# Optimization experiments

Hardware: AMD Instinct MI355X
Metric: run time of the kernel (lower is better)

The kernel has to match this reference:

```python
import jax, jax.numpy as jnp
import numpy as np

STRIDE = 8
D_STATE = 16
D_CONV = 4
DT_RANK = 8
NB = 2            # mamba blocks per direction
B, F_IN, L_IN = 2, 256, 250
F_OUT = 128
KSIZE = 16
L_OUT = (L_IN - 1) * STRIDE + KSIZE   # 2008
D_INNER = 2 * F_OUT                   # 256
LN_EPS = 1e-5


def setup_inputs() -> dict:
    key = jax.random.key(0)
    ks = jax.random.split(key, 12)
    s = 0.05
    return {
        'x': jax.random.normal(ks[0], (B, F_IN, L_IN), jnp.float32),
        'skip': jax.random.normal(ks[1], (B, F_OUT, L_OUT), jnp.float32),
        'res_for': jnp.zeros((1,), jnp.float32),
        'res_back': jnp.zeros((1,), jnp.float32),
        'convT_w': jax.random.normal(ks[2], (F_IN, F_OUT, KSIZE), jnp.float32) * s,
        'convT_b': jnp.zeros((F_OUT,), jnp.float32),
        'fuse_w': jax.random.normal(ks[3], (F_OUT, 2 * F_OUT), jnp.float32) * s,
        'fuse_b': jnp.zeros((F_OUT,), jnp.float32),
        'norm_w': jnp.ones((2, NB, F_OUT), jnp.float32),
        'norm_b': jnp.zeros((2, NB, F_OUT), jnp.float32),
        'in_proj_w': jax.random.normal(ks[4], (2, NB, 2 * D_INNER, F_OUT), jnp.float32) * s,
        'conv_w': jax.random.normal(ks[5], (2, NB, D_INNER, 1, D_CONV), jnp.float32) * s,
        'conv_b': jnp.zeros((2, NB, D_INNER), jnp.float32),
        'x_proj_w': jax.random.normal(ks[6], (2, NB, DT_RANK + 2 * D_STATE, D_INNER), jnp.float32) * s,
        'dt_proj_w': jax.random.normal(ks[7], (2, NB, D_INNER, DT_RANK), jnp.float32) * s,
        'dt_proj_b': jax.random.uniform(ks[8], (2, NB, D_INNER), jnp.float32, -4.0, -2.0),
        'A_log': jnp.broadcast_to(jnp.log(jnp.arange(1, D_STATE + 1, dtype=jnp.float32)), (2, NB, D_INNER, D_STATE)) + jnp.zeros((2, NB, D_INNER, D_STATE), jnp.float32),
        'D_skip': jnp.ones((2, NB, D_INNER), jnp.float32),
        'out_proj_w': jax.random.normal(ks[9], (2, NB, F_OUT, D_INNER), jnp.float32) * s,
    }


def _layernorm(x, w, b):
    mu = x.mean(-1, keepdims=True)
    var = ((x - mu) ** 2).mean(-1, keepdims=True)
    return (x - mu) * jax.lax.rsqrt(var + LN_EPS) * w + b


def _mamba_mixer(x, p):
    # x: [B,L,D] -> [B,L,D]
    Bb, L, _ = x.shape
    xz = jnp.einsum('bld,ed->ble', x, p['in_proj_w'])          # [B,L,2*d_in]
    xc, z = xz[..., :D_INNER], xz[..., D_INNER:]
    # causal depthwise conv1d (pad left d_conv-1)
    conv = jax.lax.conv_general_dilated(
        xc.transpose(0, 2, 1), p['conv_w'], (1,), [(D_CONV - 1, 0)],
        feature_group_count=D_INNER, dimension_numbers=('NCH', 'OIH', 'NCH'))
    xc = jax.nn.silu(conv + p['conv_b'][None, :, None]).transpose(0, 2, 1)  # [B,L,d_in]
    xdbl = jnp.einsum('bld,ed->ble', xc, p['x_proj_w'])        # [B,L,dt_rank+2N]
    dt = xdbl[..., :DT_RANK]
    Bm = xdbl[..., DT_RANK:DT_RANK + D_STATE]                  # [B,L,N]
    Cm = xdbl[..., DT_RANK + D_STATE:]                         # [B,L,N]
    delta = jax.nn.softplus(jnp.einsum('blr,dr->bld', dt, p['dt_proj_w']) + p['dt_proj_b'])
    A = -jnp.exp(p['A_log'])                                   # [d_in,N]

    def step(h, inp):
        d_t, B_t, C_t, u_t = inp                               # [B,d_in],[B,N],[B,N],[B,d_in]
        dA = jnp.exp(d_t[..., None] * A)                       # [B,d_in,N]
        h = dA * h + (d_t * u_t)[..., None] * B_t[:, None, :]
        y = jnp.einsum('bdn,bn->bd', h, C_t)
        return h, y

    h0 = jnp.zeros((Bb, D_INNER, D_STATE), xc.dtype)
    _, ys = jax.lax.scan(step, h0, (delta.transpose(1, 0, 2), Bm.transpose(1, 0, 2),
                                    Cm.transpose(1, 0, 2), xc.transpose(1, 0, 2)))
    y = ys.transpose(1, 0, 2) + xc * p['D_skip']               # [B,L,d_in]
    y = y * jax.nn.silu(z)
    return jnp.einsum('bld,od->blo', y, p['out_proj_w'])


def _mamba_stack(xseq, params, d):
    # prenorm residual blocks, as in mamba_ssm Block (fused_add_norm=False, LayerNorm)
    residual = None
    for i in range(NB):
        p = {k: params[k][d, i] for k in ('norm_w', 'norm_b', 'in_proj_w', 'conv_w', 'conv_b',
                                          'x_proj_w', 'dt_proj_w', 'dt_proj_b', 'A_log', 'D_skip', 'out_proj_w')}
        residual = xseq if residual is None else xseq + residual
        xseq = _mamba_mixer(_layernorm(residual, p['norm_w'], p['norm_b']), p)
    return xseq + residual


def _conv_transpose1d(x, w, b, stride):
    # torch ConvTranspose1d: x [B,Cin,L], w [Cin,Cout,K]
    K = w.shape[-1]
    w_t = jnp.flip(w, -1).transpose(1, 0, 2)                   # [Cout,Cin,K]
    y = jax.lax.conv_general_dilated(x, w_t, (1,), [(K - 1, K - 1)],
                                     lhs_dilation=(stride,),
                                     dimension_numbers=('NCH', 'OIH', 'NCH'))
    return y + b[None, :, None]


def _forward(x, skip, convT_w, convT_b, fuse_w, fuse_b, params):
    h = jax.nn.silu(_conv_transpose1d(x, convT_w, convT_b, STRIDE))
    pad = skip.shape[2] - h.shape[2]
    if pad > 0:
        h = jnp.pad(h, ((0, 0), (0, 0), (0, pad)))
    h = jnp.concatenate([skip, h], axis=1)                     # [B,2*F_OUT,L]
    h = jax.nn.silu(jnp.einsum('bcl,oc->bol', h, fuse_w) + fuse_b[None, :, None])
    xs = h.transpose(0, 2, 1)                                  # [B,L,F_OUT]
    xf = _mamba_stack(xs, params, 0)
    xb = jnp.flip(_mamba_stack(jnp.flip(xs, 1), params, 1), 1)
    return (xf + xb).transpose(0, 2, 1)                        # [B,F_OUT,L]


def reference(x, skip, res_for, res_back, convT_w, convT_b, fuse_w, fuse_b,
              norm_w, norm_b, in_proj_w, conv_w, conv_b, x_proj_w,
              dt_proj_w, dt_proj_b, A_log, D_skip, out_proj_w):
    params = dict(norm_w=norm_w, norm_b=norm_b, in_proj_w=in_proj_w, conv_w=conv_w,
                  conv_b=conv_b, x_proj_w=x_proj_w, dt_proj_w=dt_proj_w, dt_proj_b=dt_proj_b,
                  A_log=A_log, D_skip=D_skip, out_proj_w=out_proj_w)
    return _forward(x, skip, convT_w, convT_b, fuse_w, fuse_b, params)
```

## Files before the change

kernel.cpp:

```cpp
#include <hip/hip_runtime.h>
#include <hip/hip_bf16.h>
#include <math.h>

#define B_    2
#define FIN_  256
#define LIN_  250
#define F_    128
#define K_    16
#define ST_   8
#define L_    2008
#define DI_   256
#define DS_   16
#define RK_   8
#define CV_   4
#define NBLK_ 2
#define NC_   32
#define CL_   63
#define RL_   ((size_t)B_ * L_)

__device__ __forceinline__ float silu_f(float x) {
    return x / (1.f + __expf(-x));
}
__device__ __forceinline__ float softplus_f(float x) {
    return (x > 20.f) ? x : log1pf(__expf(x));
}
__device__ __forceinline__ float dot4(float4 a, float4 b) {
    return a.x * b.x + a.y * b.y + a.z * b.z + a.w * b.w;
}

#define PREP_N (524288 + 32768 + 262144 + 262144 + 65536)
__global__ void prep_k(const float* __restrict__ convT_w, const float* __restrict__ fuse_w,
                       const float* __restrict__ in_proj, const float* __restrict__ out_proj,
                       const float* __restrict__ x_proj,
                       float* __restrict__ W2p, float* __restrict__ fwTp,
                       float* __restrict__ ipTp, float* __restrict__ opTp,
                       float* __restrict__ xpTp) {
    size_t g = (size_t)blockIdx.x * 256 + threadIdx.x;
    if (g >= PREP_N) return;
    if (g < 524288) {
        int ccq = g >> 12, rr = g & 4095;
        int po = rr >> 2, i = rr & 3;
        int cc = ccq * 4 + i;
        int p = po >> 7, o = po & 127;
        int c = cc & 255, k = (cc < 256) ? p : p + 8;
        W2p[g] = convT_w[(size_t)c * 2048 + o * 16 + k];
        return;
    }
    g -= 524288;
    if (g < 32768) {
        int cq = g >> 9, rr = g & 511;
        int o = rr >> 2, i = rr & 3;
        fwTp[g] = fuse_w[(size_t)o * 256 + cq * 4 + i];
        return;
    }
    g -= 32768;
    if (g < 262144) {
        int db = g >> 16, r = g & 65535;
        int cq = r >> 11, rr = r & 2047;
        int e = rr >> 2, i = rr & 3;
        ipTp[g] = in_proj[(size_t)db * 65536 + e * 128 + cq * 4 + i];
        return;
    }
    g -= 262144;
    if (g < 262144) {
        int db = g >> 15, r = g & 32767;
        int cq = r >> 9, rr = r & 511;
        int o = rr >> 2, i = rr & 3;
        opTp[g] = out_proj[(size_t)db * 32768 + o * 256 + cq * 4 + i];
        return;
    }
    g -= 262144;
    {
        int db = g >> 14, r = g & 16383;
        int cq = r >> 8, rr = r & 255;
        int e = rr >> 2, i = rr & 3;
        xpTp[g] = (e < 40) ? x_proj[(size_t)db * 10240 + e * 256 + cq * 4 + i] : 0.f;
    }
}

__global__ void __launch_bounds__(256) convt4_k(
        const float* __restrict__ x, const float* __restrict__ W2p,
        const float* __restrict__ bias, float* __restrict__ hT) {
    int j0 = blockIdx.x * 4, nt = blockIdx.y, b = blockIdx.z;
    int po = nt * 256 + threadIdx.x;
    int p = po >> 7, o = po & 127;

    __shared__ float xr[5][264];

    for (int idx = threadIdx.x; idx < 5 * 256; idx += 256) {
        int i = idx >> 8, c = idx & 255;
        int j = j0 - 1 + i;
        xr[i][c] = (j >= 0 && j < LIN_) ? x[((size_t)b * FIN_ + c) * LIN_ + j] : 0.f;
    }
    __syncthreads();

    float acc[4] = {0.f, 0.f, 0.f, 0.f};
    const float4* W4 = (const float4*)W2p;

    for (int ccq = 0; ccq < 64; ++ccq) {
        float4 w1 = W4[(size_t)ccq * 1024 + po];
        float4 w2 = W4[(size_t)(ccq + 64) * 1024 + po];
        float4 xv[5];
        #pragma unroll
        for (int i = 0; i < 5; ++i) xv[i] = *(const float4*)&xr[i][ccq * 4];
        #pragma unroll
        for (int jj = 0; jj < 4; ++jj)
            acc[jj] += dot4(xv[jj + 1], w1) + dot4(xv[jj], w2);
    }
    float bo = bias[o];
    #pragma unroll
    for (int jj = 0; jj < 4; ++jj) {
        int j = j0 + jj;
        if (j <= 250) {
            int t = 8 * j + p;
            hT[((size_t)b * L_ + t) * F_ + o] = silu_f(acc[jj] + bo);
        }
    }
}

__global__ void __launch_bounds__(256) fuse4_k(
        const float* __restrict__ skip, const float* __restrict__ hT,
        const float* __restrict__ fwTp, const float* __restrict__ fb,
        float* __restrict__ xs) {
    int l0 = blockIdx.x * 8, b = blockIdx.y;
    int tid = threadIdx.x;

    __shared__ float ss[8][264];

    for (int idx = tid; idx < 128 * 8; idx += 256) {
        int c = idx >> 3, ll = idx & 7;
        ss[ll][c] = skip[((size_t)b * F_ + c) * L_ + l0 + ll];
    }
    for (int idx = tid; idx < 8 * 128; idx += 256) {
        int ll = idx >> 7, c = idx & 127;
        ss[ll][128 + c] = hT[((size_t)b * L_ + l0 + ll) * F_ + c];
    }
    __syncthreads();

    int o = tid & 127, lh = tid >> 7;
    float acc[4] = {0.f, 0.f, 0.f, 0.f};
    const float4* W4 = (const float4*)fwTp;

    for (int cq = 0; cq < 64; ++cq) {
        float4 w = W4[cq * 128 + o];
        #pragma unroll
        for (int rr = 0; rr < 4; ++rr)
            acc[rr] += dot4(*(const float4*)&ss[lh * 4 + rr][cq * 4], w);
    }
    float bo = fb[o];
    #pragma unroll
    for (int rr = 0; rr < 4; ++rr) {
        int l = l0 + lh * 4 + rr;
        float v = silu_f(acc[rr] + bo);
        xs[((size_t)b * L_ + l) * F_ + o] = v;
        xs[(RL_ + (size_t)b * L_ + (L_ - 1 - l)) * F_ + o] = v;
    }
}

__global__ void __launch_bounds__(256) ln4_k(
        const float* __restrict__ X, const float* __restrict__ nw,
        const float* __restrict__ nb_, const float* __restrict__ ipTp,
        float* __restrict__ XZ, int blk) {
    int rt = blockIdx.x, nt = blockIdx.y, d = blockIdx.z;
    int n0 = nt * 128;
    size_t rbase = (size_t)rt * 32;
    int tid = threadIdx.x, lane = tid & 63, wid = tid >> 6;
    int db = d * NBLK_ + blk;

    __shared__ float us[32][132];

    int wi0 = db * F_;
    for (int rr = 0; rr < 8; ++rr) {
        int r = wid * 8 + rr;
        size_t row = rbase + r;
        float2 v = make_float2(0.f, 0.f);
        if (row < RL_)
            v = *(const float2*)(X + ((size_t)d * RL_ + row) * F_ + lane * 2);
        float s1 = v.x + v.y, s2 = v.x * v.x + v.y * v.y;
        for (int off = 32; off; off >>= 1) {
            s1 += __shfl_xor(s1, off);
            s2 += __shfl_xor(s2, off);
        }
        float mu = s1 * (1.f / F_);
        float var = s2 * (1.f / F_) - mu * mu;
        float rstd = rsqrtf(var + 1e-5f);
        int c = lane * 2;
        us[r][c]     = (v.x - mu) * rstd * nw[wi0 + c]     + nb_[wi0 + c];
        us[r][c + 1] = (v.y - mu) * rstd * nw[wi0 + c + 1] + nb_[wi0 + c + 1];
    }
    __syncthreads();

    int o = tid & 127, rh = tid >> 7;
    float acc[16];
    #pragma unroll
    for (int i = 0; i < 16; ++i) acc[i] = 0.f;
    const float4* W4 = (const float4*)(ipTp + (size_t)db * 65536);

    for (int cq = 0; cq < 32; ++cq) {
        float4 w = W4[cq * 512 + n0 + o];
        #pragma unroll
        for (int rr = 0; rr < 16; ++rr)
            acc[rr] += dot4(*(const float4*)&us[rh * 16 + rr][cq * 4], w);
    }
    for (int rr = 0; rr < 16; ++rr) {
        size_t row = rbase + rh * 16 + rr;
        if (row < RL_)
            XZ[((size_t)d * RL_ + row) * (2 * DI_) + n0 + o] = acc[rr];
    }
}

__global__ void __launch_bounds__(256) dwxdt_k(
        const float* __restrict__ XZ, const float* __restrict__ cw,
        const float* __restrict__ cb, const float* __restrict__ xpTp,
        const float* __restrict__ dtw, const float* __restrict__ dtb,
        float* __restrict__ XC, float* __restrict__ BCM,
        float* __restrict__ DELTA, int blk) {
    int rt = blockIdx.x, d = blockIdx.y;
    int tid = threadIdx.x;
    size_t rbase = (size_t)rt * 16;
    int db = d * NBLK_ + blk;

    __shared__ float xzs[19][264];
    __shared__ float xcs[16][264];
    __shared__ float dts[16][8];

    for (int idx = tid; idx < 19 * 256; idx += 256) {
        int s = idx >> 8;
        int c = idx & 255;
        long g = (long)rbase - 3 + s;
        xzs[s][c] = (g >= 0) ? XZ[((size_t)d * RL_ + g) * (2 * DI_) + c] : 0.f;
    }
    __syncthreads();

    {
        int ch = tid;
        int wi = db * DI_ + ch;
        float w0 = cw[(size_t)wi * CV_ + 0], w1 = cw[(size_t)wi * CV_ + 1];
        float w2 = cw[(size_t)wi * CV_ + 2], w3 = cw[(size_t)wi * CV_ + 3];
        float bias = cb[wi];
        #pragma unroll 4
        for (int r = 0; r < 16; ++r) {
            size_t row = rbase + r;
            int b = (row >= L_) ? 1 : 0;
            int l = (int)(row - (size_t)b * L_);
            int s = r + 3;
            float acc = bias + xzs[s][ch] * w3;
            if (l - 1 >= 0) acc += xzs[s - 1][ch] * w2;
            if (l - 2 >= 0) acc += xzs[s - 2][ch] * w1;
            if (l - 3 >= 0) acc += xzs[s - 3][ch] * w0;
            float v = silu_f(acc);
            xcs[r][ch] = v;
            XC[((size_t)d * RL_ + row) * DI_ + ch] = v;
        }
    }
    __syncthreads();

    {
        int e = tid & 63, rg = tid >> 6;
        float acc[4] = {0.f, 0.f, 0.f, 0.f};
        const float4* W4 = (const float4*)(xpTp + (size_t)db * 16384);
        for (int cq = 0; cq < 64; ++cq) {
            float4 w = W4[cq * 64 + e];
            #pragma unroll
            for (int rr = 0; rr < 4; ++rr)
                acc[rr] += dot4(*(const float4*)&xcs[rg * 4 + rr][cq * 4], w);
        }
        if (e < RK_) {
            #pragma unroll
            for (int rr = 0; rr < 4; ++rr) dts[rg * 4 + rr][e] = acc[rr];
        } else if (e < RK_ + 2 * DS_) {
            #pragma unroll
            for (int rr = 0; rr < 4; ++rr) {
                size_t row = rbase + rg * 4 + rr;
                BCM[((size_t)d * RL_ + row) * 32 + (e - RK_)] = acc[rr];
            }
        }
    }
    __syncthreads();

    {
        int ch = tid;
        int wi = db * DI_ + ch;
        float dwv[RK_];
        #pragma unroll
        for (int k = 0; k < RK_; ++k) dwv[k] = dtw[(size_t)wi * RK_ + k];
        float bias = dtb[wi];
        #pragma unroll 4
        for (int rr = 0; rr < 16; ++rr) {
            size_t row = rbase + rr;
            float acc = bias;
            #pragma unroll
            for (int k = 0; k < RK_; ++k) acc += dts[rr][k] * dwv[k];
            DELTA[((size_t)d * RL_ + row) * DI_ + ch] = softplus_f(acc);
        }
    }
}

__global__ void __launch_bounds__(256) scanA_k(
        float* __restrict__ DELTA, const float* __restrict__ XC,
        const float* __restrict__ BCM, const float* __restrict__ A_log,
        float* __restrict__ Y, float* __restrict__ hpart,
        float* __restrict__ dsum, int blk) {
    int d = blockIdx.z, cnk = blockIdx.y;
    int chunit0 = blockIdx.x * 16;
    int chl = threadIdx.x >> 4, n = threadIdx.x & 15;
    int b = chunit0 >> 8, ch0 = chunit0 & 255;
    int ch = ch0 + chl;
    int t0 = cnk * CL_;
    int nt = L_ - t0 < CL_ ? L_ - t0 : CL_;

    __shared__ float dt_s[CL_][16];
    __shared__ float u_s[CL_][16];
    __shared__ float bc_s[CL_][32];

    size_t rowbase = (size_t)d * RL_ + (size_t)b * L_ + t0;
    for (int idx = threadIdx.x; idx < CL_ * 16; idx += 256) {
        int t = idx >> 4, c = idx & 15;
        float dv = 0.f, uv = 0.f;
        if (t < nt) {
            dv = DELTA[(rowbase + t) * DI_ + ch0 + c];
            uv = XC[(rowbase + t) * DI_ + ch0 + c];
        }
        dt_s[t][c] = dv; u_s[t][c] = uv;
    }
    for (int idx = threadIdx.x; idx < CL_ * 32; idx += 256) {
        int t = idx >> 5, m = idx & 31;
        bc_s[t][m] = (t < nt) ? BCM[(rowbase + t) * 32 + m] : 0.f;
    }
    __syncthreads();

    float A = -__expf(A_log[((size_t)(d * NBLK_ + blk) * DI_ + ch) * DS_ + n]);
    float h = 0.f, cum = 0.f;
    for (int t = 0; t < nt; ++t) {
        float dt = dt_s[t][chl];
        float u  = u_s[t][chl];
        float Bt = bc_s[t][n];
        float Ct = bc_s[t][16 + n];
        cum += dt;
        h = __expf(dt * A) * h + dt * u * Bt;
        float yp = h * Ct;
        yp += __shfl_xor(yp, 1);
        yp += __shfl_xor(yp, 2);
        yp += __shfl_xor(yp, 4);
        yp += __shfl_xor(yp, 8);
        if (n == 0) {
            Y[(rowbase + t) * DI_ + ch] = yp;
            DELTA[(rowbase + t) * DI_ + ch] = cum;
        }
    }
    size_t cb = (size_t)(d * B_ + b) * NC_ + cnk;
    hpart[cb * (DI_ * DS_) + ch * DS_ + n] = h;
    if (n == 0) dsum[cb * DI_ + ch] = cum;
}

__global__ void scanB_k(float* __restrict__ hpart, const float* __restrict__ dsum,
                        const float* __restrict__ A_log, int blk) {
    int d = blockIdx.y;
    int idx = blockIdx.x * 256 + threadIdx.x;
    int b = idx >> 12, ch = (idx >> 4) & 255, n = idx & 15;
    float A = -__expf(A_log[((size_t)(d * NBLK_ + blk) * DI_ + ch) * DS_ + n]);
    float h = 0.f;
    for (int c = 0; c < NC_; ++c) {
        size_t cb = (size_t)(d * B_ + b) * NC_ + c;
        size_t hi = cb * (DI_ * DS_) + ch * DS_ + n;
        float hc = hpart[hi];
        hpart[hi] = h;
        h = __expf(A * dsum[cb * DI_ + ch]) * h + hc;
    }
}

__global__ void __launch_bounds__(256) fixD_k(
        const float* __restrict__ DELTA , const float* __restrict__ BCM,
        const float* __restrict__ A_log, const float* __restrict__ hcarry,
        float* __restrict__ Y, int blk) {
    int d = blockIdx.z, cnk = blockIdx.y + 1;
    int chunit0 = blockIdx.x * 16;
    int b = chunit0 >> 8, ch0 = chunit0 & 255;
    int chl = threadIdx.x & 15, tg = threadIdx.x >> 4;
    int ch = ch0 + chl;
    int t0 = cnk * CL_;
    int nt = L_ - t0 < CL_ ? L_ - t0 : CL_;

    __shared__ float cum_s[CL_][17];
    __shared__ float c_s[CL_][17];
    __shared__ float hin_s[16][16];

    size_t rowbase = (size_t)d * RL_ + (size_t)b * L_ + t0;
    for (int idx = threadIdx.x; idx < CL_ * 16; idx += 256) {
        int t = idx >> 4, c = idx & 15;
        float cv = 0.f, Cv = 0.f;
        if (t < nt) {
            cv = DELTA[(rowbase + t) * DI_ + ch0 + c];
            Cv = BCM[(rowbase + t) * 32 + 16 + c];
        }
        cum_s[t][c] = cv; c_s[t][c] = Cv;
    }
    {
        size_t cb = ((size_t)(d * B_ + b) * NC_ + cnk) * (DI_ * DS_);
        int cl = threadIdx.x >> 4, n = threadIdx.x & 15;
        hin_s[cl][n] = hcarry[cb + (ch0 + cl) * DS_ + n];
    }
    __syncthreads();

    float An[16], Kn[16];
    const float* Ab = A_log + ((size_t)(d * NBLK_ + blk) * DI_ + ch) * DS_;
    #pragma unroll
    for (int n = 0; n < 16; ++n) {
        An[n] = -__expf(Ab[n]);
        Kn[n] = hin_s[chl][n];
    }
    #pragma unroll
    for (int tt = 0; tt < 4; ++tt) {
        int t = tg * 4 + tt;
        if (t < nt) {
            float cum = cum_s[t][chl];
            float corr = 0.f;
            #pragma unroll
            for (int n = 0; n < 16; ++n)
                corr += c_s[t][n] * Kn[n] * __expf(An[n] * cum);
            Y[(rowbase + t) * DI_ + ch] += corr;
        }
    }
}

__global__ void __launch_bounds__(256) gate4_k(
        const float* __restrict__ Y, const float* __restrict__ XC,
        const float* __restrict__ XZ, const float* __restrict__ Dsk,
        const float* __restrict__ opTp, const float* __restrict__ resid_in,
        float* __restrict__ outp, int blk) {
    int rt = blockIdx.x, d = blockIdx.y;
    int tid = threadIdx.x;
    size_t rbase = (size_t)rt * 16;
    int db = d * NBLK_ + blk;

    __shared__ float yg[16][264];

    {
        int c = tid;
        float Dc = Dsk[(size_t)db * DI_ + c];
        #pragma unroll 4
        for (int r = 0; r < 16; ++r) {
            size_t ri = (size_t)d * RL_ + rbase + r;
            float z = XZ[ri * (2 * DI_) + DI_ + c];
            yg[r][c] = (Y[ri * DI_ + c] + XC[ri * DI_ + c] * Dc) * silu_f(z);
        }
    }
    __syncthreads();

    int o = tid & 127, rh = tid >> 7;
    float acc[8];
    #pragma unroll
    for (int i = 0; i < 8; ++i) acc[i] = 0.f;
    const float4* W4 = (const float4*)(opTp + (size_t)db * 32768);

    for (int cq = 0; cq < 64; ++cq) {
        float4 w = W4[cq * 128 + o];
        #pragma unroll
        for (int rr = 0; rr < 8; ++rr)
            acc[rr] += dot4(*(const float4*)&yg[rh * 8 + rr][cq * 4], w);
    }
    for (int rr = 0; rr < 8; ++rr) {
        size_t row = rbase + rh * 8 + rr;
        size_t ri = (size_t)d * RL_ + row;
        float v = acc[rr];
        if (resid_in) v += resid_in[ri * F_ + o];
        outp[ri * F_ + o] = v;
    }
}

__global__ void combine2_k(const float* __restrict__ cur, const float* __restrict__ res1,
                           float* __restrict__ out) {
    int l0 = blockIdx.x * 64, b = blockIdx.y;
    int tid = threadIdx.x;
    __shared__ float s[64][129];
    for (int idx = tid; idx < 64 * 128; idx += 256) {
        int ll = idx >> 7, o = idx & 127;
        int l = l0 + ll;
        if (l < L_) {
            size_t rf = ((size_t)b * L_ + l) * F_ + o;
            size_t rb = (RL_ + (size_t)b * L_ + (L_ - 1 - l)) * F_ + o;
            s[ll][o] = cur[rf] + res1[rf] + cur[rb] + res1[rb];
        }
    }
    __syncthreads();
    for (int idx = tid; idx < 64 * 128; idx += 256) {
        int o = idx >> 6, ll = idx & 63;
        int l = l0 + ll;
        if (l < L_) out[((size_t)b * F_ + o) * L_ + l] = s[ll][o];
    }
}

extern "C" void kernel_launch(void* const* d_in, const int* in_sizes, int n_in,
                              void* d_out, int out_size, void* d_ws, size_t ws_size,
                              hipStream_t stream) {
    const float* x        = (const float*)d_in[0];
    const float* skip     = (const float*)d_in[1];
    const float* convT_w  = (const float*)d_in[4];
    const float* convT_b  = (const float*)d_in[5];
    const float* fuse_w   = (const float*)d_in[6];
    const float* fuse_b   = (const float*)d_in[7];
    const float* norm_w   = (const float*)d_in[8];
    const float* norm_b   = (const float*)d_in[9];
    const float* in_proj  = (const float*)d_in[10];
    const float* conv_w   = (const float*)d_in[11];
    const float* conv_b   = (const float*)d_in[12];
    const float* x_proj   = (const float*)d_in[13];
    const float* dt_projw = (const float*)d_in[14];
    const float* dt_projb = (const float*)d_in[15];
    const float* A_log    = (const float*)d_in[16];
    const float* D_skip   = (const float*)d_in[17];
    const float* out_proj = (const float*)d_in[18];
    float* out = (float*)d_out;

    float* w = (float*)d_ws;
    size_t off = 0;
    auto alloc = [&](size_t n) { float* p = w + off; off += n; return p; };
    float* hT      = alloc((size_t)B_ * L_ * F_);
    float* W2p     = alloc(524288);
    float* fwTp    = alloc(32768);
    float* ipTp    = alloc(262144);
    float* opTp    = alloc(262144);
    float* xpTp    = alloc(65536);
    float* xs      = alloc(2 * RL_ * F_);
    float* cur     = alloc(2 * RL_ * F_);
    float* res1    = alloc(2 * RL_ * F_);
    float* xz      = alloc(2 * RL_ * (2 * DI_));
    float* xc      = alloc(2 * RL_ * DI_);
    float* dl      = alloc(2 * RL_ * DI_);
    float* bcm     = alloc(2 * RL_ * 32);
    float* yb      = alloc(2 * RL_ * DI_);
    float* hp   = hT;
    float* dsum = hT + 524288;
    (void)ws_size; (void)in_sizes; (void)n_in; (void)out_size;

    prep_k<<<(PREP_N + 255) / 256, 256, 0, stream>>>(convT_w, fuse_w, in_proj, out_proj,
                                                     x_proj, W2p, fwTp, ipTp, opTp, xpTp);
    convt4_k<<<dim3(63, 4, 2), 256, 0, stream>>>(x, W2p, convT_b, hT);
    fuse4_k<<<dim3(251, 2), 256, 0, stream>>>(skip, hT, fwTp, fuse_b, xs);

    for (int blk = 0; blk < NBLK_; ++blk) {
        const float* Xin = (blk == 0) ? xs : res1;
        ln4_k<<<dim3(126, 4, 2), 256, 0, stream>>>(Xin, norm_w, norm_b, ipTp, xz, blk);
        dwxdt_k<<<dim3(251, 2), 256, 0, stream>>>(xz, conv_w, conv_b, xpTp,
                                                  dt_projw, dt_projb, xc, bcm, dl, blk);
        scanA_k<<<dim3(32, NC_, 2), 256, 0, stream>>>(dl, xc, bcm, A_log, yb, hp, dsum, blk);
        scanB_k<<<dim3(32, 2), 256, 0, stream>>>(hp, dsum, A_log, blk);
        fixD_k<<<dim3(32, NC_ - 1, 2), 256, 0, stream>>>(dl, bcm, A_log, hp, yb, blk);
        if (blk == 0)
            gate4_k<<<dim3(251, 2), 256, 0, stream>>>(yb, xc, xz, D_skip, opTp, xs, res1, 0);
        else
            gate4_k<<<dim3(251, 2), 256, 0, stream>>>(yb, xc, xz, D_skip, opTp, nullptr, cur, 1);
    }

    combine2_k<<<dim3(32, 2), 256, 0, stream>>>(cur, res1, out);
}
```

Baseline: 454.2 us.

## Re-tile GEMM kernels to multiple outputs per thread and double scan chunk count

The convT, fuse, LN+in_proj and gate GEMM kernels now compute two or four output columns per thread, so each shared-memory activation load is reused across more weights. The LN kernel now produces all 512 in_proj outputs per block over 16 rows instead of splitting N across grid.y, which removes the repeated LayerNorm work. The scan chunking goes from 32 chunks of 63 steps to 64 chunks of 32 steps, shortening the serial per-chunk work but making the carry pass longer. The dsum scratch buffer is moved into `cur` to fit the larger carry arrays, which is safe only because `cur` is written later, and more accumulators per thread raise register pressure.

```diff
diff --git a/kernel.cpp b/kernel.cpp
--- a/kernel.cpp
+++ b/kernel.cpp
@@ -14,8 +14,8 @@
 #define RK_   8
 #define CV_   4
 #define NBLK_ 2
-#define NC_   32
-#define CL_   63
+#define NC_   64
+#define CL_   32
 #define RL_   ((size_t)B_ * L_)
 
 __device__ __forceinline__ float silu_f(float x) {
@@ -78,11 +78,11 @@
     }
 }
 
-__global__ void __launch_bounds__(256) convt4_k(
+__global__ void __launch_bounds__(256) convt5_k(
         const float* __restrict__ x, const float* __restrict__ W2p,
         const float* __restrict__ bias, float* __restrict__ hT) {
     int j0 = blockIdx.x * 4, nt = blockIdx.y, b = blockIdx.z;
-    int po = nt * 256 + threadIdx.x;
+    int po = nt * 512 + threadIdx.x;
     int p = po >> 7, o = po & 127;
 
     __shared__ float xr[5][264];
@@ -94,31 +94,36 @@
     }
     __syncthreads();
 
-    float acc[4] = {0.f, 0.f, 0.f, 0.f};
+    float acca[4] = {0.f, 0.f, 0.f, 0.f};
+    float accb[4] = {0.f, 0.f, 0.f, 0.f};
     const float4* W4 = (const float4*)W2p;
 
     for (int ccq = 0; ccq < 64; ++ccq) {
-        float4 w1 = W4[(size_t)ccq * 1024 + po];
-        float4 w2 = W4[(size_t)(ccq + 64) * 1024 + po];
+        float4 wa1 = W4[(size_t)ccq * 1024 + po];
+        float4 wb1 = W4[(size_t)ccq * 1024 + po + 256];
+        float4 wa2 = W4[(size_t)(ccq + 64) * 1024 + po];
+        float4 wb2 = W4[(size_t)(ccq + 64) * 1024 + po + 256];
         float4 xv[5];
         #pragma unroll
         for (int i = 0; i < 5; ++i) xv[i] = *(const float4*)&xr[i][ccq * 4];
         #pragma unroll
-        for (int jj = 0; jj < 4; ++jj)
-            acc[jj] += dot4(xv[jj + 1], w1) + dot4(xv[jj], w2);
+        for (int jj = 0; jj < 4; ++jj) {
+            acca[jj] += dot4(xv[jj + 1], wa1) + dot4(xv[jj], wa2);
+            accb[jj] += dot4(xv[jj + 1], wb1) + dot4(xv[jj], wb2);
+        }
     }
     float bo = bias[o];
     #pragma unroll
     for (int jj = 0; jj < 4; ++jj) {
         int j = j0 + jj;
         if (j <= 250) {
-            int t = 8 * j + p;
-            hT[((size_t)b * L_ + t) * F_ + o] = silu_f(acc[jj] + bo);
-        }
-    }
-}
-
-__global__ void __launch_bounds__(256) fuse4_k(
+            hT[((size_t)b * L_ + 8 * j + p) * F_ + o]     = silu_f(acca[jj] + bo);
+            hT[((size_t)b * L_ + 8 * j + p + 2) * F_ + o] = silu_f(accb[jj] + bo);
+        }
+    }
+}
+
+__global__ void __launch_bounds__(256) fuse5_k(
         const float* __restrict__ skip, const float* __restrict__ hT,
         const float* __restrict__ fwTp, const float* __restrict__ fb,
         float* __restrict__ xs) {
@@ -137,45 +142,50 @@
     }
     __syncthreads();
 
-    int o = tid & 127, lh = tid >> 7;
-    float acc[4] = {0.f, 0.f, 0.f, 0.f};
+    int o2 = tid & 63, rg = tid >> 6;
+    float acca[2] = {0.f, 0.f}, accb[2] = {0.f, 0.f};
     const float4* W4 = (const float4*)fwTp;
 
     for (int cq = 0; cq < 64; ++cq) {
-        float4 w = W4[cq * 128 + o];
+        float4 wa = W4[cq * 128 + o2];
+        float4 wb = W4[cq * 128 + o2 + 64];
         #pragma unroll
-        for (int rr = 0; rr < 4; ++rr)
-            acc[rr] += dot4(*(const float4*)&ss[lh * 4 + rr][cq * 4], w);
-    }
-    float bo = fb[o];
-    #pragma unroll
-    for (int rr = 0; rr < 4; ++rr) {
-        int l = l0 + lh * 4 + rr;
-        float v = silu_f(acc[rr] + bo);
-        xs[((size_t)b * L_ + l) * F_ + o] = v;
-        xs[(RL_ + (size_t)b * L_ + (L_ - 1 - l)) * F_ + o] = v;
-    }
-}
-
-__global__ void __launch_bounds__(256) ln4_k(
+        for (int rr = 0; rr < 2; ++rr) {
+            float4 s = *(const float4*)&ss[rg * 2 + rr][cq * 4];
+            acca[rr] += dot4(s, wa);
+            accb[rr] += dot4(s, wb);
+        }
+    }
+    float ba = fb[o2], bb = fb[o2 + 64];
+    #pragma unroll
+    for (int rr = 0; rr < 2; ++rr) {
+        int l = l0 + rg * 2 + rr;
+        float va = silu_f(acca[rr] + ba);
+        float vb = silu_f(accb[rr] + bb);
+        size_t rf = ((size_t)b * L_ + l) * F_;
+        size_t rb = (RL_ + (size_t)b * L_ + (L_ - 1 - l)) * F_;
+        xs[rf + o2] = va;       xs[rf + o2 + 64] = vb;
+        xs[rb + o2] = va;       xs[rb + o2 + 64] = vb;
+    }
+}
+
+__global__ void __launch_bounds__(256) ln5_k(
         const float* __restrict__ X, const float* __restrict__ nw,
         const float* __restrict__ nb_, const float* __restrict__ ipTp,
         float* __restrict__ XZ, int blk) {
-    int rt = blockIdx.x, nt = blockIdx.y, d = blockIdx.z;
-    int n0 = nt * 128;
-    size_t rbase = (size_t)rt * 32;
+    int rt = blockIdx.x, d = blockIdx.y;
+    size_t rbase = (size_t)rt * 16;
     int tid = threadIdx.x, lane = tid & 63, wid = tid >> 6;
     int db = d * NBLK_ + blk;
 
-    __shared__ float us[32][132];
+    __shared__ float us[16][132];
 
     int wi0 = db * F_;
-    for (int rr = 0; rr < 8; ++rr) {
-        int r = wid * 8 + rr;
+    #pragma unroll
+    for (int rr = 0; rr < 4; ++rr) {
+        int r = wid * 4 + rr;
         size_t row = rbase + r;
-        float2 v = make_float2(0.f, 0.f);
-        if (row < RL_)
-            v = *(const float2*)(X + ((size_t)d * RL_ + row) * F_ + lane * 2);
+        float2 v = *(const float2*)(X + ((size_t)d * RL_ + row) * F_ + lane * 2);
         float s1 = v.x + v.y, s2 = v.x * v.x + v.y * v.y;
         for (int off = 32; off; off >>= 1) {
             s1 += __shfl_xor(s1, off);
@@ -191,21 +201,33 @@
     __syncthreads();
 
     int o = tid & 127, rh = tid >> 7;
-    float acc[16];
-    #pragma unroll
-    for (int i = 0; i < 16; ++i) acc[i] = 0.f;
+    float acc0[8], acc1[8], acc2[8], acc3[8];
+    #pragma unroll
+    for (int i = 0; i < 8; ++i) { acc0[i] = acc1[i] = acc2[i] = acc3[i] = 0.f; }
     const float4* W4 = (const float4*)(ipTp + (size_t)db * 65536);
 
     for (int cq = 0; cq < 32; ++cq) {
-        float4 w = W4[cq * 512 + n0 + o];
+        float4 w0 = W4[cq * 512 + o];
+        float4 w1 = W4[cq * 512 + o + 128];
+        float4 w2 = W4[cq * 512 + o + 256];
+        float4 w3 = W4[cq * 512 + o + 384];
         #pragma unroll
-        for (int rr = 0; rr < 16; ++rr)
-            acc[rr] += dot4(*(const float4*)&us[rh * 16 + rr][cq * 4], w);
-    }
-    for (int rr = 0; rr < 16; ++rr) {
-        size_t row = rbase + rh * 16 + rr;
-        if (row < RL_)
-            XZ[((size_t)d * RL_ + row) * (2 * DI_) + n0 + o] = acc[rr];
+        for (int rr = 0; rr < 8; ++rr) {
+            float4 u = *(const float4*)&us[rh * 8 + rr][cq * 4];
+            acc0[rr] += dot4(u, w0);
+            acc1[rr] += dot4(u, w1);
+            acc2[rr] += dot4(u, w2);
+            acc3[rr] += dot4(u, w3);
+        }
+    }
+    #pragma unroll
+    for (int rr = 0; rr < 8; ++rr) {
+        size_t row = rbase + rh * 8 + rr;
+        float* dst = XZ + ((size_t)d * RL_ + row) * (2 * DI_);
+        dst[o]       = acc0[rr];
+        dst[o + 128] = acc1[rr];
+        dst[o + 256] = acc2[rr];
+        dst[o + 384] = acc3[rr];
     }
 }
 
@@ -307,7 +329,7 @@
     int b = chunit0 >> 8, ch0 = chunit0 & 255;
     int ch = ch0 + chl;
     int t0 = cnk * CL_;
-    int nt = L_ - t0 < CL_ ? L_ - t0 : CL_;
+    int nt = L_ - t0; if (nt > CL_) nt = CL_;
 
     __shared__ float dt_s[CL_][16];
     __shared__ float u_s[CL_][16];
@@ -379,7 +401,7 @@
     int chl = threadIdx.x & 15, tg = threadIdx.x >> 4;
     int ch = ch0 + chl;
     int t0 = cnk * CL_;
-    int nt = L_ - t0 < CL_ ? L_ - t0 : CL_;
+    int nt = L_ - t0; if (nt > CL_) nt = CL_;
 
     __shared__ float cum_s[CL_][17];
     __shared__ float c_s[CL_][17];
@@ -397,8 +419,8 @@
     }
     {
         size_t cb = ((size_t)(d * B_ + b) * NC_ + cnk) * (DI_ * DS_);
-        int cl = threadIdx.x >> 4, n = threadIdx.x & 15;
-        hin_s[cl][n] = hcarry[cb + (ch0 + cl) * DS_ + n];
+        int cl = threadIdx.x >> 4, nn = threadIdx.x & 15;
+        hin_s[cl][nn] = hcarry[cb + (ch0 + cl) * DS_ + nn];
     }
     __syncthreads();
 
@@ -410,8 +432,8 @@
         Kn[n] = hin_s[chl][n];
     }
     #pragma unroll
-    for (int tt = 0; tt < 4; ++tt) {
-        int t = tg * 4 + tt;
+    for (int tt = 0; tt < 2; ++tt) {
+        int t = tg * 2 + tt;
         if (t < nt) {
             float cum = cum_s[t][chl];
             float corr = 0.f;
@@ -423,7 +445,7 @@
     }
 }
 
-__global__ void __launch_bounds__(256) gate4_k(
+__global__ void __launch_bounds__(256) gate5_k(
         const float* __restrict__ Y, const float* __restrict__ XC,
         const float* __restrict__ XZ, const float* __restrict__ Dsk,
         const float* __restrict__ opTp, const float* __restrict__ resid_in,
@@ -447,24 +469,31 @@
     }
     __syncthreads();
 
-    int o = tid & 127, rh = tid >> 7;
-    float acc[8];
-    #pragma unroll
-    for (int i = 0; i < 8; ++i) acc[i] = 0.f;
+    int o2 = tid & 63, rg = tid >> 6;
+    float acca[4] = {0.f, 0.f, 0.f, 0.f};
+    float accb[4] = {0.f, 0.f, 0.f, 0.f};
     const float4* W4 = (const float4*)(opTp + (size_t)db * 32768);
 
     for (int cq = 0; cq < 64; ++cq) {
-        float4 w = W4[cq * 128 + o];
+        float4 wa = W4[cq * 128 + o2];
+        float4 wb = W4[cq * 128 + o2 + 64];
         #pragma unroll
-        for (int rr = 0; rr < 8; ++rr)
-            acc[rr] += dot4(*(const float4*)&yg[rh * 8 + rr][cq * 4], w);
-    }
-    for (int rr = 0; rr < 8; ++rr) {
-        size_t row = rbase + rh * 8 + rr;
-        size_t ri = (size_t)d * RL_ + row;
-        float v = acc[rr];
-        if (resid_in) v += resid_in[ri * F_ + o];
-        outp[ri * F_ + o] = v;
+        for (int rr = 0; rr < 4; ++rr) {
+            float4 u = *(const float4*)&yg[rg * 4 + rr][cq * 4];
+            acca[rr] += dot4(u, wa);
+            accb[rr] += dot4(u, wb);
+        }
+    }
+    #pragma unroll
+    for (int rr = 0; rr < 4; ++rr) {
+        size_t ri = (size_t)d * RL_ + rbase + rg * 4 + rr;
+        float va = acca[rr], vb = accb[rr];
+        if (resid_in) {
+            va += resid_in[ri * F_ + o2];
+            vb += resid_in[ri * F_ + o2 + 64];
+        }
+        outp[ri * F_ + o2]      = va;
+        outp[ri * F_ + o2 + 64] = vb;
     }
 }
 
@@ -530,26 +559,26 @@
     float* bcm     = alloc(2 * RL_ * 32);
     float* yb      = alloc(2 * RL_ * DI_);
     float* hp   = hT;
-    float* dsum = hT + 524288;
+    float* dsum = cur;
     (void)ws_size; (void)in_sizes; (void)n_in; (void)out_size;
 
     prep_k<<<(PREP_N + 255) / 256, 256, 0, stream>>>(convT_w, fuse_w, in_proj, out_proj,
                                                      x_proj, W2p, fwTp, ipTp, opTp, xpTp);
-    convt4_k<<<dim3(63, 4, 2), 256, 0, stream>>>(x, W2p, convT_b, hT);
-    fuse4_k<<<dim3(251, 2), 256, 0, stream>>>(skip, hT, fwTp, fuse_b, xs);
+    convt5_k<<<dim3(63, 2, 2), 256, 0, stream>>>(x, W2p, convT_b, hT);
+    fuse5_k<<<dim3(251, 2), 256, 0, stream>>>(skip, hT, fwTp, fuse_b, xs);
 
     for (int blk = 0; blk < NBLK_; ++blk) {
         const float* Xin = (blk == 0) ? xs : res1;
-        ln4_k<<<dim3(126, 4, 2), 256, 0, stream>>>(Xin, norm_w, norm_b, ipTp, xz, blk);
+        ln5_k<<<dim3(251, 2), 256, 0, stream>>>(Xin, norm_w, norm_b, ipTp, xz, blk);
         dwxdt_k<<<dim3(251, 2), 256, 0, stream>>>(xz, conv_w, conv_b, xpTp,
                                                   dt_projw, dt_projb, xc, bcm, dl, blk);
         scanA_k<<<dim3(32, NC_, 2), 256, 0, stream>>>(dl, xc, bcm, A_log, yb, hp, dsum, blk);
         scanB_k<<<dim3(32, 2), 256, 0, stream>>>(hp, dsum, A_log, blk);
         fixD_k<<<dim3(32, NC_ - 1, 2), 256, 0, stream>>>(dl, bcm, A_log, hp, yb, blk);
         if (blk == 0)
-            gate4_k<<<dim3(251, 2), 256, 0, stream>>>(yb, xc, xz, D_skip, opTp, xs, res1, 0);
+            gate5_k<<<dim3(251, 2), 256, 0, stream>>>(yb, xc, xz, D_skip, opTp, xs, res1, 0);
         else
-            gate4_k<<<dim3(251, 2), 256, 0, stream>>>(yb, xc, xz, D_skip, opTp, nullptr, cur, 1);
+            gate5_k<<<dim3(251, 2), 256, 0, stream>>>(yb, xc, xz, D_skip, opTp, nullptr, cur, 1);
     }
 
     combine2_k<<<dim3(32, 2), 256, 0, stream>>>(cur, res1, out);
```

New measurement: 439.3 us. 3.3% less time.
